# Kernel optimization log

Measured on AMD Instinct MI355X. Metric: run time of the kernel, lower is better.

The kernel has to match this reference:

```python
import jax, jax.numpy as jnp
import numpy as np

N_U, N_D = 64, 64
N_E = N_U + N_D
N_A = 32
N_SV, N_PV = 512, 64
# n1 = [4*N_A, N_SV, N_SV, N_SV]; n2 = [4, N_PV, N_PV, N_PV]


def setup_inputs() -> dict:
    key = jax.random.key(0)
    ks = jax.random.split(key, 32)
    n1 = [4 * N_A, N_SV, N_SV, N_SV]
    n2 = [4, N_PV, N_PV, N_PV]
    d = {}
    d['r'] = jax.random.normal(ks[0], (N_E, 3), jnp.float32)
    d['a'] = jax.random.normal(ks[1], (N_A, 3), jnp.float32)
    i = 2
    for l in range(3):
        fin = 3 * n1[l] + 2 * n2[l]
        d[f'V{l}_w'] = jax.random.normal(ks[i], (fin, n1[l + 1]), jnp.float32) / np.float32(np.sqrt(fin)); i += 1
        d[f'V{l}_b'] = jax.random.normal(ks[i], (n1[l + 1],), jnp.float32); i += 1
        d[f'W{l}_w'] = jax.random.normal(ks[i], (n2[l], n2[l + 1]), jnp.float32) / np.float32(np.sqrt(n2[l])); i += 1
        d[f'W{l}_b'] = jax.random.normal(ks[i], (n2[l + 1],), jnp.float32); i += 1
    fin = 3 * N_SV + 2 * N_PV
    d['after_w'] = jax.random.normal(ks[i], (fin, N_SV), jnp.float32) / np.float32(np.sqrt(fin)); i += 1
    d['after_b'] = jax.random.normal(ks[i], (N_SV,), jnp.float32); i += 1
    d['vhu_w'] = jax.random.normal(ks[i], (N_SV, N_SV // 2), jnp.float32) / np.float32(np.sqrt(N_SV)); i += 1
    d['vhu_b'] = jax.random.normal(ks[i], (N_SV // 2,), jnp.float32); i += 1
    d['vhd_w'] = jax.random.normal(ks[i], (N_SV, N_SV // 2), jnp.float32) / np.float32(np.sqrt(N_SV)); i += 1
    d['vhd_b'] = jax.random.normal(ks[i], (N_SV // 2,), jnp.float32); i += 1
    d['wu_w'] = jax.random.normal(ks[i], (N_SV // 2, N_U), jnp.float32) / np.float32(np.sqrt(N_SV // 2)); i += 1
    d['wu_b'] = jax.random.normal(ks[i], (N_U,), jnp.float32); i += 1
    d['wd_w'] = jax.random.normal(ks[i], (N_SV // 2, N_D), jnp.float32) / np.float32(np.sqrt(N_SV // 2)); i += 1
    d['wd_b'] = jax.random.normal(ks[i], (N_D,), jnp.float32); i += 1
    return d


def _fb_block(s_v, p_v):
    # s_v: (N_E, f_s), p_v: (N_E, N_E, f_p)
    s_u_mean = jnp.tile(s_v[:N_U].mean(0)[None, :], (N_E, 1))
    s_d_mean = jnp.tile(s_v[N_U:].mean(0)[None, :], (N_E, 1))
    p_u_mean = p_v[:N_U].mean(0)  # (N_E, f_p)
    p_d_mean = p_v[N_U:].mean(0)
    return jnp.concatenate([s_u_mean, s_d_mean, p_u_mean, p_d_mean, s_v], axis=-1)


def _forward(r, a, Vw, Vb, Ww, Wb, after_w, after_b, vhu_w, vhu_b, vhd_w, vhd_b, wu_w, wu_b, wd_w, wd_b):
    eye = jnp.eye(N_E, dtype=r.dtype)[:, :, None]
    ra = r[:, None, :] - a[None, :, :]                       # (N_E, N_A, 3)
    ra_len = jnp.linalg.norm(ra, axis=-1, keepdims=True)     # (N_E, N_A, 1)
    rr = r[None, :, :] - r[:, None, :]                       # (N_E, N_E, 3)
    rr_len = jnp.linalg.norm(rr + eye, axis=-1, keepdims=True) * (1.0 - eye)
    s_v = jnp.concatenate([ra, ra_len], axis=-1).reshape(N_E, -1)  # (N_E, 4*N_A)
    p_v = jnp.concatenate([rr, rr_len], axis=-1)                   # (N_E, N_E, 4)
    for vw, vb, ww, wb in zip(Vw, Vb, Ww, Wb):
        s_in = _fb_block(s_v, p_v)
        # NOTE: torch residual `s_v if s_v.shape[-1]==n_sv` never fires here:
        # fb_block output width is 3*n1+2*n2 != n_sv, so it adds zeros.
        s_v = jnp.tanh(s_in @ vw + vb)
        p_new = jnp.tanh(p_v @ ww + wb)
        p_v = p_new + (p_v if p_v.shape[-1] == N_PV else 0.0)
    s_in = _fb_block(s_v, p_v)
    s_v = jnp.tanh(s_in @ after_w + after_b)  # (N_E, N_SV); residual again never fires
    s_u = s_v[:N_U] @ vhu_w + vhu_b
    s_d = s_v[N_U:] @ vhd_w + vhd_b
    s_wu = s_u @ wu_w + wu_b   # (N_U, N_U)
    s_wd = s_d @ wd_w + wd_b   # (N_D, N_D)
    exp_u = jnp.linalg.norm(ra[:N_U], axis=-1, keepdims=True)  # (N_U, N_A, 1)
    exp_d = jnp.linalg.norm(ra[N_U:], axis=-1, keepdims=True)
    orb_u = (s_wu * jnp.exp(-exp_u).sum(axis=1))[None]  # (1, N_U, N_U)
    orb_d = (s_wd * jnp.exp(-exp_d).sum(axis=1))[None]
    # logabssumdet for two (1,n,n) matrices with n>1: no 1x1 dets.
    sgn_u, ld_u = jnp.linalg.slogdet(orb_u)
    sgn_d, ld_d = jnp.linalg.slogdet(orb_d)
    sign = sgn_u * sgn_d
    logdet = ld_u + ld_d        # (1,)
    maxlogdet = logdet.max()
    psi = (sign * jnp.exp(logdet - maxlogdet)).sum()
    return jnp.log(jnp.abs(psi)) + maxlogdet  # scalar log|psi|


def reference(r, a, V0_w, V0_b, V1_w, V1_b, V2_w, V2_b, W0_w, W0_b, W1_w, W1_b, W2_w, W2_b,
              after_w, after_b, vhu_w, vhu_b, vhd_w, vhd_b, wu_w, wu_b, wd_w, wd_b):
    Vw, Vb = [V0_w, V1_w, V2_w], [V0_b, V1_b, V2_b]
    Ww, Wb = [W0_w, W1_w, W2_w], [W0_b, W1_b, W2_b]
    return _forward(r, a, Vw, Vb, Ww, Wb, after_w, after_b,
                    vhu_w, vhu_b, vhd_w, vhd_b, wu_w, wu_b, wd_w, wd_b)
```

## Files before the change

kernel.cpp:

```cpp
#include <hip/hip_runtime.h>
#include <math.h>

#define NSV 512

__device__ void pchain_role(int b, const float* __restrict__ r,
                            const float* __restrict__ apos,
                            const float* __restrict__ W0w, const float* __restrict__ W0b,
                            const float* __restrict__ W1w, const float* __restrict__ W1b,
                            const float* __restrict__ W2w, const float* __restrict__ W2b,
                            float* __restrict__ expv,
                            float* __restrict__ pme1, float* __restrict__ pme2,
                            float* __restrict__ pme3, float* sh)
{
    float* rL    = sh;
    float* W0l   = sh + 384;
    float* aposL = sh + 640;
    float* shex  = sh + 736;
    float* p0c   = sh + 768;
    float* PA    = sh + 1024;
    float* Wbuf  = sh + 5376;
    const int j  = b >> 1, sp = b & 1;
    const int t  = threadIdx.x;
    const int i  = t >> 3;
    const int o0 = (t & 7) * 8;

    if (t < 384) rL[t] = r[t];
    else if (t < 480) aposL[t - 384] = apos[t - 384];
    for (int idx = t; idx < 4096; idx += 512) Wbuf[idx] = W1w[idx];
    if (t < 256) W0l[t] = W0w[t];
    __syncthreads();

    const float rjx = rL[j*3+0], rjy = rL[j*3+1], rjz = rL[j*3+2];
    if (t < 64) {
        const int ii = sp*64 + t;
        float dx = rjx - rL[ii*3+0], dy = rjy - rL[ii*3+1], dz = rjz - rL[ii*3+2];
        float len = (ii == j) ? 0.f : sqrtf(dx*dx + dy*dy + dz*dz);
        p0c[t*4+0]=dx; p0c[t*4+1]=dy; p0c[t*4+2]=dz; p0c[t*4+3]=len;
    } else if (sp == 0 && t < 96) {
        const int k = t - 64;
        float dx = rjx - aposL[k*3+0], dy = rjy - aposL[k*3+1], dz = rjz - aposL[k*3+2];
        shex[k] = expf(-sqrtf(dx*dx + dy*dy + dz*dz));
    }
    __syncthreads();

    {
        const float x0=p0c[i*4+0], x1=p0c[i*4+1], x2=p0c[i*4+2], x3=p0c[i*4+3];
        #pragma unroll
        for (int k = 0; k < 8; ++k) {
            const int o = o0 + k;
            float a = W0b[o];
            a = fmaf(x0, W0l[o],     a);
            a = fmaf(x1, W0l[64+o],  a);
            a = fmaf(x2, W0l[128+o], a);
            a = fmaf(x3, W0l[192+o], a);
            PA[i*68+o] = tanhf(a);
        }
    }
    if (sp == 0 && t == 4) {
        float s = 0.f;
        #pragma unroll 8
        for (int k = 0; k < 32; ++k) s += shex[k];
        expv[j] = s;
    }
    __syncthreads();

    if (t < 64) {
        float s = 0.f;
        #pragma unroll 8
        for (int k = 0; k < 64; ++k) s += PA[k*68 + t];
        pme1[j*128 + sp*64 + t] = s * 0.015625f;
    }
    float acc[8], res[8];
    const float* pa = PA + i*68;
    {
        #pragma unroll
        for (int k = 0; k < 8; ++k) acc[k] = W1b[o0+k];
        #pragma unroll 4
        for (int c = 0; c < 64; ++c) {
            const float av = pa[c];
            const float* wr = Wbuf + c*64 + o0;
            float4 wa = *reinterpret_cast<const float4*>(wr);
            float4 wb = *reinterpret_cast<const float4*>(wr+4);
            acc[0]=fmaf(av,wa.x,acc[0]); acc[1]=fmaf(av,wa.y,acc[1]);
            acc[2]=fmaf(av,wa.z,acc[2]); acc[3]=fmaf(av,wa.w,acc[3]);
            acc[4]=fmaf(av,wb.x,acc[4]); acc[5]=fmaf(av,wb.y,acc[5]);
            acc[6]=fmaf(av,wb.z,acc[6]); acc[7]=fmaf(av,wb.w,acc[7]);
        }
        #pragma unroll
        for (int k = 0; k < 8; ++k) res[k] = pa[o0+k];
    }
    __syncthreads();
    #pragma unroll
    for (int k = 0; k < 8; ++k) PA[i*68+o0+k] = tanhf(acc[k]) + res[k];
    __syncthreads();

    if (t < 64) {
        float s = 0.f;
        #pragma unroll 8
        for (int k = 0; k < 64; ++k) s += PA[k*68 + t];
        pme2[j*128 + sp*64 + t] = s * 0.015625f;
    }
    for (int idx = t; idx < 4096; idx += 512) Wbuf[idx] = W2w[idx];
    __syncthreads();

    {
        #pragma unroll
        for (int k = 0; k < 8; ++k) acc[k] = W2b[o0+k];
        #pragma unroll 4
        for (int c = 0; c < 64; ++c) {
            const float av = pa[c];
            const float* wr = Wbuf + c*64 + o0;
            float4 wa = *reinterpret_cast<const float4*>(wr);
            float4 wb = *reinterpret_cast<const float4*>(wr+4);
            acc[0]=fmaf(av,wa.x,acc[0]); acc[1]=fmaf(av,wa.y,acc[1]);
            acc[2]=fmaf(av,wa.z,acc[2]); acc[3]=fmaf(av,wa.w,acc[3]);
            acc[4]=fmaf(av,wb.x,acc[4]); acc[5]=fmaf(av,wb.y,acc[5]);
            acc[6]=fmaf(av,wb.z,acc[6]); acc[7]=fmaf(av,wb.w,acc[7]);
        }
        #pragma unroll
        for (int k = 0; k < 8; ++k) res[k] = pa[o0+k];
    }
    __syncthreads();
    #pragma unroll
    for (int k = 0; k < 8; ++k) PA[i*68+o0+k] = tanhf(acc[k]) + res[k];
    __syncthreads();

    if (t < 64) {
        float s = 0.f;
        #pragma unroll 8
        for (int k = 0; k < 64; ++k) s += PA[k*68 + t];
        pme3[j*128 + sp*64 + t] = s * 0.015625f;
    }
}

__device__ void a0_role(int ab, const float* __restrict__ r,
                        const float* __restrict__ apos,
                        const float* __restrict__ V0w, const float* __restrict__ V0b,
                        float* __restrict__ svA, float* __restrict__ psA, float* sh)
{
    constexpr int KP = 136, KP2 = 68;
    float* As    = sh;
    float* smL   = sh + 544;
    float* red   = sh + 800;
    float* t1L   = sh + 1312;
    float* rL    = sh + 1376;
    float* aposL = sh + 1760;
    const int t  = threadIdx.x;
    const int et = ab >> 3, e0 = et * 4;
    const int o0 = (ab & 7) * 64;
    const int ol = t & 63, o = o0 + ol;
    const int wv = t >> 6;

    if (t < 384) rL[t] = r[t];
    else if (t < 480) aposL[t - 384] = apos[t - 384];
    __syncthreads();

    if (t < 128) {
        const int e_l = t >> 5, k = t & 31;
        const int e = e0 + e_l;
        float dx = rL[e*3+0]-aposL[k*3+0], dy = rL[e*3+1]-aposL[k*3+1],
              dz = rL[e*3+2]-aposL[k*3+2];
        float len = sqrtf(dx*dx + dy*dy + dz*dz);
        float* dst = As + e_l*KP + 8 + k*4;
        dst[0]=dx; dst[1]=dy; dst[2]=dz; dst[3]=len;
    } else if (t < 160) {
        const int q = t - 128;
        const int e_l = q >> 3, outp = q & 7;
        const int spin = outp >> 2, c = outp & 3;
        const int e = e0 + e_l;
        const float ex = rL[e*3+0], ey = rL[e*3+1], ez = rL[e*3+2];
        float s = 0.f;
        for (int i2 = 0; i2 < 64; ++i2) {
            const int ii = spin*64 + i2;
            float dx = ex - rL[ii*3+0], dy = ey - rL[ii*3+1], dz = ez - rL[ii*3+2];
            float v = (c==0)?dx:(c==1)?dy:(c==2)?dz:
                      ((ii==e)?0.f:sqrtf(dx*dx+dy*dy+dz*dz));
            s += v;
        }
        As[e_l*KP + outp] = s * 0.015625f;
    }
    {
        const int outp = t >> 1, half = t & 1;
        const int spin = outp >> 7, cc = outp & 127, a_i = cc >> 2, d = cc & 3;
        const float ax = aposL[a_i*3+0], ay = aposL[a_i*3+1], az = aposL[a_i*3+2];
        float s = 0.f;
        #pragma unroll 8
        for (int q = 0; q < 32; ++q) {
            const int e = spin*64 + half*32 + q;
            float dx = rL[e*3+0]-ax, dy = rL[e*3+1]-ay, dz = rL[e*3+2]-az;
            float len = sqrtf(dx*dx + dy*dy + dz*dz);
            s += (d==0)?dx:(d==1)?dy:(d==2)?dz:len;
        }
        red[t] = s;
    }
    __syncthreads();
    if (t < 256) smL[t] = (red[2*t] + red[2*t+1]) * 0.015625f;
    __syncthreads();

    {
        float a1 = 0.f;
        const float* Wp = V0w + (size_t)(wv*32)*NSV + o;
        const float* mp = smL + wv*32;
        #pragma unroll 8
        for (int k = 0; k < 32; ++k) a1 = fmaf(mp[k], Wp[(size_t)k*NSV], a1);
        red[wv*64 + ol] = a1;
    }
    __syncthreads();
    if (t < 64) {
        float s = V0b[o0 + t];
        #pragma unroll
        for (int g = 0; g < 8; ++g) s += red[g*64 + t];
        t1L[t] = s;
    }
    __syncthreads();

    const int e_l = wv & 3, kh = wv >> 2;
    {
        float a2 = (kh == 0) ? t1L[ol] : 0.f;
        const float* Ap = As + e_l*KP + kh*KP2;
        const float* Wp = V0w + (size_t)(256 + kh*KP2)*NSV + o;
        #pragma unroll 16
        for (int k = 0; k < KP2; ++k)
            a2 = fmaf(Ap[k], Wp[(size_t)k*NSV], a2);
        red[wv*64 + ol] = a2;
    }
    __syncthreads();
    float v = 0.f;
    if (t < 256) {
        v = tanhf(red[(t>>6)*64 + (t&63)] + red[((t>>6)+4)*64 + (t&63)]);
        svA[(size_t)(e0 + (t>>6))*NSV + o0 + (t&63)] = v;
    }
    __syncthreads();
    if (t < 256) red[t] = v;
    __syncthreads();
    if (t < 64) {
        float s = red[t] + red[64+t] + red[128+t] + red[192+t];
        psA[(size_t)et*NSV + o0 + t] = s;
    }
}

__device__ void headc_role(int g, const float* __restrict__ vh,
                           const float* __restrict__ wu,
                           float* __restrict__ Cdst, float* sh)
{
    float* wuL = sh;
    float* vhL = sh + 4096;
    const int t = threadIdx.x;
    const int o2 = t & 63, wq = t >> 6;
    const int f0 = g * 16;
    float a0 = 0.f, a1 = 0.f;
    for (int hc = 0; hc < 4; ++hc) {
        __syncthreads();
        for (int idx = t; idx < 4096; idx += 512)
            wuL[idx] = wu[(size_t)(hc*64 + (idx>>6))*64 + (idx&63)];
        for (int idx = t; idx < 1024; idx += 512)
            vhL[idx] = vh[(size_t)(f0 + (idx>>6))*256 + hc*64 + (idx&63)];
        __syncthreads();
        #pragma unroll 8
        for (int h = 0; h < 64; ++h) {
            const float wuv = wuL[h*64 + o2];
            a0 = fmaf(vhL[wq*64 + h],     wuv, a0);
            a1 = fmaf(vhL[(wq+8)*64 + h], wuv, a1);
        }
    }
    Cdst[(size_t)(f0 + wq)*64 + o2]     = a0;
    Cdst[(size_t)(f0 + wq + 8)*64 + o2] = a1;
}

__device__ void cb_role(const float* __restrict__ vhb, const float* __restrict__ wu,
                        const float* __restrict__ wub, float* __restrict__ cbdst,
                        float* sh)
{
    const int t = threadIdx.x;
    const int o2 = t & 63, wq = t >> 6;
    float acc = 0.f;
    #pragma unroll
    for (int k = 0; k < 32; ++k) {
        const int h = wq*32 + k;
        acc = fmaf(vhb[h], wu[(size_t)h*64 + o2], acc);
    }
    sh[t] = acc;
    __syncthreads();
    if (t < 64) {
        float s = wub[t];
        #pragma unroll
        for (int g = 0; g < 8; ++g) s += sh[g*64 + t];
        cbdst[t] = s;
    }
}

__global__ __launch_bounds__(512)
void front_kernel(const float* __restrict__ r, const float* __restrict__ apos,
                  const float* __restrict__ V0w, const float* __restrict__ V0b,
                  const float* __restrict__ W0w, const float* __restrict__ W0b,
                  const float* __restrict__ W1w, const float* __restrict__ W1b,
                  const float* __restrict__ W2w, const float* __restrict__ W2b,
                  const float* __restrict__ vhuw, const float* __restrict__ vhub,
                  const float* __restrict__ vhdw, const float* __restrict__ vhdb,
                  const float* __restrict__ wuw,  const float* __restrict__ wub,
                  const float* __restrict__ wdw,  const float* __restrict__ wdb,
                  float* __restrict__ svA, float* __restrict__ expv,
                  float* __restrict__ pme1, float* __restrict__ pme2,
                  float* __restrict__ pme3, float* __restrict__ psA,
                  float* __restrict__ Cmat, float* __restrict__ cb)
{
    __shared__ __align__(16) float sh[9472];
    const int b = blockIdx.x;
    if (b < 256) {
        pchain_role(b, r, apos, W0w, W0b, W1w, W1b, W2w, W2b,
                    expv, pme1, pme2, pme3, sh);
    } else if (b < 512) {
        a0_role(b - 256, r, apos, V0w, V0b, svA, psA, sh);
    } else if (b < 576) {
        const int g = b - 512;
        const int spin = g >> 5;
        headc_role(g & 31, spin ? vhdw : vhuw, spin ? wdw : wuw,
                   Cmat + (size_t)spin*32768, sh);
    } else {
        const int spin = b - 576;
        cb_role(spin ? vhdb : vhub, spin ? wdw : wuw, spin ? wdb : wub,
                cb + spin*64, sh);
    }
}

template<int FS, int FP>
__global__ __launch_bounds__(512)
void a2_kernel(const float* __restrict__ svIn, const float* __restrict__ pmeIn,
               const float* __restrict__ psumIn,
               const float* __restrict__ Vw, const float* __restrict__ Vb,
               float* __restrict__ svOut, float* __restrict__ psumOut,
               float* __restrict__ orbInit, const float* __restrict__ cb)
{
    constexpr int KP  = 2*FP + FS;
    constexpr int KP2 = KP/2;
    __shared__ __align__(16) float As[4*KP];
    __shared__ __align__(16) float smL[2*FS];
    __shared__ __align__(16) float red[512];
    __shared__ float t1L[64];
    const int t  = threadIdx.x;
    if (blockIdx.x >= 256) {
        for (int idx = t; idx < 8192; idx += 512)
            orbInit[idx] = cb[(((idx >> 6) >> 6) << 6) + (idx & 63)];
        return;
    }
    const int et = blockIdx.x >> 3;
    const int e0 = et * 4;
    const int o0 = (blockIdx.x & 7) * 64;
    const int ol = t & 63;
    const int o  = o0 + ol;
    const int wv = t >> 6;

    for (int idx = t; idx < 4*2*FP; idx += 512)
        As[(idx/(2*FP))*KP + idx%(2*FP)] =
            pmeIn[(size_t)(e0 + idx/(2*FP))*(2*FP) + idx%(2*FP)];
    for (int idx = t; idx < FS; idx += 512) {
        const int row = idx / (FS/4), c4 = idx % (FS/4);
        *reinterpret_cast<float4*>(&As[row*KP + 2*FP + c4*4]) =
            *reinterpret_cast<const float4*>(&svIn[(size_t)(e0+row)*FS + c4*4]);
    }
    for (int idx = t; idx < 2*FS; idx += 512) {
        const int col = (idx < FS) ? idx : idx - FS;
        const int r0  = (idx < FS) ? 0 : 16;
        const float* base = psumIn + (size_t)r0*NSV + col;
        float s = 0.f;
        #pragma unroll
        for (int k = 0; k < 16; ++k) s += base[(size_t)k*NSV];
        smL[idx] = s * 0.015625f;
    }
    __syncthreads();

    {
        constexpr int TI = (2*FS)/8;
        float a1 = 0.f;
        const float* Wp = Vw + (size_t)(wv*TI)*NSV + o;
        const float* mp = smL + wv*TI;
        #pragma unroll 8
        for (int k = 0; k < TI; ++k) a1 = fmaf(mp[k], Wp[(size_t)k*NSV], a1);
        red[wv*64 + ol] = a1;
    }
    __syncthreads();
    if (t < 64) {
        float s = Vb[o0 + t];
        #pragma unroll
        for (int g = 0; g < 8; ++g) s += red[g*64 + t];
        t1L[t] = s;
    }
    __syncthreads();

    const int e_l = wv & 3, kh = wv >> 2;
    {
        float a2 = (kh == 0) ? t1L[ol] : 0.f;
        const float* Ap = As + e_l*KP + kh*KP2;
        const float* Wp = Vw + (size_t)(2*FS + kh*KP2)*NSV + o;
        #pragma unroll 16
        for (int k = 0; k < KP2; ++k)
            a2 = fmaf(Ap[k], Wp[(size_t)k*NSV], a2);
        red[wv*64 + ol] = a2;
    }
    __syncthreads();
    float v = 0.f;
    if (t < 256) {
        v = tanhf(red[(t>>6)*64 + (t&63)] + red[((t>>6)+4)*64 + (t&63)]);
        svOut[(size_t)(e0 + (t>>6))*NSV + o0 + (t&63)] = v;
    }
    if (psumOut) {
        __syncthreads();
        if (t < 256) red[t] = v;
        __syncthreads();
        if (t < 64) {
            float s = red[t] + red[64+t] + red[128+t] + red[192+t];
            psumOut[(size_t)et*NSV + o0 + t] = s;
        }
    }
}

__global__ __launch_bounds__(512)
void a3h_kernel(const float* __restrict__ svIn, const float* __restrict__ pmeIn,
                const float* __restrict__ psumIn,
                const float* __restrict__ Vw, const float* __restrict__ Vb,
                const float* __restrict__ Cmat, float* __restrict__ orb)
{
    constexpr int FS = 512, FP = 64;
    constexpr int KP  = 2*FP + FS;
    constexpr int KP2 = KP/2;
    __shared__ __align__(16) float As[4*KP];
    __shared__ __align__(16) float smL[2*FS];
    __shared__ __align__(16) float red[512];
    __shared__ float t1L[64];
    const int t  = threadIdx.x;
    const int et = blockIdx.x >> 3;
    const int e0 = et * 4;
    const int o0 = (blockIdx.x & 7) * 64;
    const int ol = t & 63;
    const int o  = o0 + ol;
    const int wv = t >> 6;

    for (int idx = t; idx < 4*2*FP; idx += 512)
        As[(idx/(2*FP))*KP + idx%(2*FP)] =
            pmeIn[(size_t)(e0 + idx/(2*FP))*(2*FP) + idx%(2*FP)];
    for (int idx = t; idx < FS; idx += 512) {
        const int row = idx / (FS/4), c4 = idx % (FS/4);
        *reinterpret_cast<float4*>(&As[row*KP + 2*FP + c4*4]) =
            *reinterpret_cast<const float4*>(&svIn[(size_t)(e0+row)*FS + c4*4]);
    }
    for (int idx = t; idx < 2*FS; idx += 512) {
        const int col = (idx < FS) ? idx : idx - FS;
        const int r0  = (idx < FS) ? 0 : 16;
        const float* base = psumIn + (size_t)r0*NSV + col;
        float s = 0.f;
        #pragma unroll
        for (int k = 0; k < 16; ++k) s += base[(size_t)k*NSV];
        smL[idx] = s * 0.015625f;
    }
    __syncthreads();

    {
        constexpr int TI = (2*FS)/8;
        float a1 = 0.f;
        const float* Wp = Vw + (size_t)(wv*TI)*NSV + o;
        const float* mp = smL + wv*TI;
        #pragma unroll 8
        for (int k = 0; k < TI; ++k) a1 = fmaf(mp[k], Wp[(size_t)k*NSV], a1);
        red[wv*64 + ol] = a1;
    }
    __syncthreads();
    if (t < 64) {
        float s = Vb[o0 + t];
        #pragma unroll
        for (int g = 0; g < 8; ++g) s += red[g*64 + t];
        t1L[t] = s;
    }
    __syncthreads();

    const int e_l = wv & 3, kh = wv >> 2;
    {
        float a2 = (kh == 0) ? t1L[ol] : 0.f;
        const float* Ap = As + e_l*KP + kh*KP2;
        const float* Wp = Vw + (size_t)(2*FS + kh*KP2)*NSV + o;
        #pragma unroll 16
        for (int k = 0; k < KP2; ++k)
            a2 = fmaf(Ap[k], Wp[(size_t)k*NSV], a2);
        red[wv*64 + ol] = a2;
    }
    __syncthreads();
    float v = 0.f;
    if (t < 256)
        v = tanhf(red[(t>>6)*64 + (t&63)] + red[((t>>6)+4)*64 + (t&63)]);
    __syncthreads();
    if (t < 256) smL[t] = v;
    __syncthreads();
    if (t < 256) {
        const int el2 = t >> 6, o2 = t & 63;
        const int spin = et >> 4;
        const float* Cp = Cmat + (size_t)spin*32768 + (size_t)o0*64 + o2;
        const float* sp = smL + el2*64;
        float acc = 0.f;
        #pragma unroll 8
        for (int f = 0; f < 64; ++f)
            acc = fmaf(sp[f], Cp[(size_t)f*64], acc);
        atomicAdd(&orb[(size_t)(e0 + el2)*64 + o2], acc);
    }
}

__device__ __forceinline__ int imax2(int a, int b) { return a > b ? a : b; }
__device__ __forceinline__ float readlane_f(float x, int lane) {
    return __int_as_float(__builtin_amdgcn_readlane(__float_as_int(x), lane));
}

__global__ __launch_bounds__(128)
void det_kernel(const float* __restrict__ orb, const float* __restrict__ expv,
                float* __restrict__ out)
{
    __shared__ float parts[2];
    const int t = threadIdx.x;
    const int w = t >> 6;
    const int lane = t & 63;
    const float* M = orb + (size_t)w*4096 + (size_t)lane*64;
    const float ex = expv[w*64 + lane];
    float rr[64];
    #pragma unroll
    for (int j = 0; j < 64; j += 4) {
        float4 v = *reinterpret_cast<const float4*>(M + j);
        rr[j]=v.x*ex; rr[j+1]=v.y*ex; rr[j+2]=v.z*ex; rr[j+3]=v.w*ex;
    }
    float pv_mine = 1.f;
    bool active = true;
    #pragma unroll
    for (int k = 0; k < 64; ++k) {
        int bits = (int)(__float_as_uint(rr[k]) & 0x7FFFFFC0u);
        int v = active ? (bits | lane) : lane;
        int tmp;
        tmp = __builtin_amdgcn_update_dpp(0, v, 0xB1,  0xF, 0xF, true); v = imax2(v, tmp);
        tmp = __builtin_amdgcn_update_dpp(0, v, 0x4E,  0xF, 0xF, true); v = imax2(v, tmp);
        tmp = __builtin_amdgcn_update_dpp(0, v, 0x141, 0xF, 0xF, true); v = imax2(v, tmp);
        tmp = __builtin_amdgcn_update_dpp(0, v, 0x140, 0xF, 0xF, true); v = imax2(v, tmp);
        tmp = __builtin_amdgcn_update_dpp(0, v, 0x142, 0xF, 0xF, true); v = imax2(v, tmp);
        tmp = __builtin_amdgcn_update_dpp(0, v, 0x143, 0xF, 0xF, true); v = imax2(v, tmp);
        const int idx = __builtin_amdgcn_readlane(v, 63) & 63;
        const float piv = readlane_f(rr[k], idx);
        pv_mine = (lane == k) ? piv : pv_mine;
        const float linv = __builtin_amdgcn_rcpf(piv);
        const float l = (active && lane != idx) ? rr[k]*linv : 0.f;
        if (lane == idx) active = false;
        #pragma unroll
        for (int j = k+1; j < 64; ++j)
            rr[j] = fmaf(-l, readlane_f(rr[j], idx), rr[j]);
    }
    float lg = logf(fabsf(pv_mine));
    #pragma unroll
    for (int off = 32; off; off >>= 1) lg += __shfl_down(lg, off);
    if (lane == 0) parts[w] = lg;
    __syncthreads();
    if (t == 0) out[0] = parts[0] + parts[1];
}

extern "C" void kernel_launch(void* const* d_in, const int* in_sizes, int n_in,
                              void* d_out, int out_size, void* d_ws, size_t ws_size,
                              hipStream_t stream)
{
    const float* r    = (const float*)d_in[0];
    const float* apos = (const float*)d_in[1];
    const float* V0w  = (const float*)d_in[2];
    const float* V0b  = (const float*)d_in[3];
    const float* W0w  = (const float*)d_in[4];
    const float* W0b  = (const float*)d_in[5];
    const float* V1w  = (const float*)d_in[6];
    const float* V1b  = (const float*)d_in[7];
    const float* W1w  = (const float*)d_in[8];
    const float* W1b  = (const float*)d_in[9];
    const float* V2w  = (const float*)d_in[10];
    const float* V2b  = (const float*)d_in[11];
    const float* W2w  = (const float*)d_in[12];
    const float* W2b  = (const float*)d_in[13];
    const float* afw  = (const float*)d_in[14];
    const float* afb  = (const float*)d_in[15];
    const float* vhuw = (const float*)d_in[16];
    const float* vhub = (const float*)d_in[17];
    const float* vhdw = (const float*)d_in[18];
    const float* vhdb = (const float*)d_in[19];
    const float* wuw  = (const float*)d_in[20];
    const float* wub  = (const float*)d_in[21];
    const float* wdw  = (const float*)d_in[22];
    const float* wdb  = (const float*)d_in[23];

    float* ws   = (float*)d_ws;
    float* svA  = ws;
    float* svB  = svA  + 65536;
    float* expv = svB  + 65536;
    float* pme1 = expv + 128;
    float* pme2 = pme1 + 16384;
    float* pme3 = pme2 + 16384;
    float* psA  = pme3 + 16384;
    float* psB  = psA  + 16384;
    float* orb  = psB  + 16384;
    float* Cmat = orb  + 8192;
    float* cb   = Cmat + 65536;

    front_kernel<<<578, 512, 0, stream>>>(r, apos, V0w, V0b, W0w, W0b,
                                          W1w, W1b, W2w, W2b,
                                          vhuw, vhub, vhdw, vhdb,
                                          wuw, wub, wdw, wdb,
                                          svA, expv, pme1, pme2, pme3, psA,
                                          Cmat, cb);
    a2_kernel<512, 64><<<257, 512, 0, stream>>>(svA, pme1, psA, V1w, V1b,
                                                svB, psB, orb, cb);
    a2_kernel<512, 64><<<256, 512, 0, stream>>>(svB, pme2, psB, V2w, V2b,
                                                svA, psA, nullptr, nullptr);
    a3h_kernel<<<256, 512, 0, stream>>>(svA, pme3, psA, afw, afb, Cmat, orb);
    det_kernel<<<1, 128, 0, stream>>>(orb, expv, (float*)d_out);
}
```

Before: 91.68 us.

## Fuse determinant into last layer kernel via last-block atomic counter

Removes the separate det_kernel launch by having every a3h block increment a global counter after its orb atomics. The last block to arrive runs the LU-based slogdet tail, reading orb through device-scope atomic loads. The counter is reset in the extra block of the first a2 kernel. This saves one kernel launch and its gap, but relies on relaxed atomics plus an explicit vmcnt wait for cross-block visibility, and the determinant now runs inside a block sized for 512 threads.

Result: slower. 94.88 us (+3.5%).

```diff
diff --git a/kernel.cpp b/kernel.cpp
--- a/kernel.cpp
+++ b/kernel.cpp
@@ -2,6 +2,12 @@
 #include <math.h>
 
 #define NSV 512
+
+__device__ __forceinline__ float2 gload2(const float* p) {
+    unsigned long long u = __hip_atomic_load((const unsigned long long*)p,
+                            __ATOMIC_RELAXED, __HIP_MEMORY_SCOPE_AGENT);
+    union { unsigned long long u; float2 f; } c; c.u = u; return c.f;
+}
 
 __device__ void pchain_role(int b, const float* __restrict__ r,
                             const float* __restrict__ apos,
@@ -329,7 +335,8 @@
                const float* __restrict__ psumIn,
                const float* __restrict__ Vw, const float* __restrict__ Vb,
                float* __restrict__ svOut, float* __restrict__ psumOut,
-               float* __restrict__ orbInit, const float* __restrict__ cb)
+               float* __restrict__ orbInit, const float* __restrict__ cb,
+               unsigned* __restrict__ cnt)
 {
     constexpr int KP  = 2*FP + FS;
     constexpr int KP2 = KP/2;
@@ -341,6 +348,9 @@
     if (blockIdx.x >= 256) {
         for (int idx = t; idx < 8192; idx += 512)
             orbInit[idx] = cb[(((idx >> 6) >> 6) << 6) + (idx & 63)];
+        if (t == 0)
+            __hip_atomic_store(cnt, 0u, __ATOMIC_RELAXED,
+                               __HIP_MEMORY_SCOPE_AGENT);
         return;
     }
     const int et = blockIdx.x >> 3;
@@ -414,11 +424,66 @@
     }
 }
 
-__global__ __launch_bounds__(512)
-void a3h_kernel(const float* __restrict__ svIn, const float* __restrict__ pmeIn,
-                const float* __restrict__ psumIn,
-                const float* __restrict__ Vw, const float* __restrict__ Vb,
-                const float* __restrict__ Cmat, float* __restrict__ orb)
+__device__ __forceinline__ int imax2(int a, int b) { return a > b ? a : b; }
+__device__ __forceinline__ float readlane_f(float x, int lane) {
+    return __int_as_float(__builtin_amdgcn_readlane(__float_as_int(x), lane));
+}
+
+__device__ void det_tail(const float* __restrict__ orb,
+                         const float* __restrict__ expv,
+                         float* __restrict__ out, float* shparts)
+{
+    const int t = threadIdx.x;
+    if (t < 128) {
+        const int w = t >> 6;
+        const int lane = t & 63;
+        const float* M = orb + (size_t)w*4096 + (size_t)lane*64;
+        const float ex = expv[w*64 + lane];
+        float rr[64];
+        #pragma unroll
+        for (int j = 0; j < 64; j += 2) {
+            float2 v = gload2(M + j);
+            rr[j] = v.x * ex; rr[j+1] = v.y * ex;
+        }
+        float pv_mine = 1.f;
+        bool active = true;
+        #pragma unroll
+        for (int k = 0; k < 64; ++k) {
+            int bits = (int)(__float_as_uint(rr[k]) & 0x7FFFFFC0u);
+            int v = active ? (bits | lane) : lane;
+            int tmp;
+            tmp = __builtin_amdgcn_update_dpp(0, v, 0xB1,  0xF, 0xF, true); v = imax2(v, tmp);
+            tmp = __builtin_amdgcn_update_dpp(0, v, 0x4E,  0xF, 0xF, true); v = imax2(v, tmp);
+            tmp = __builtin_amdgcn_update_dpp(0, v, 0x141, 0xF, 0xF, true); v = imax2(v, tmp);
+            tmp = __builtin_amdgcn_update_dpp(0, v, 0x140, 0xF, 0xF, true); v = imax2(v, tmp);
+            tmp = __builtin_amdgcn_update_dpp(0, v, 0x142, 0xF, 0xF, true); v = imax2(v, tmp);
+            tmp = __builtin_amdgcn_update_dpp(0, v, 0x143, 0xF, 0xF, true); v = imax2(v, tmp);
+            const int idx = __builtin_amdgcn_readlane(v, 63) & 63;
+            const float piv = readlane_f(rr[k], idx);
+            pv_mine = (lane == k) ? piv : pv_mine;
+            const float linv = __builtin_amdgcn_rcpf(piv);
+            const float l = (active && lane != idx) ? rr[k]*linv : 0.f;
+            if (lane == idx) active = false;
+            #pragma unroll
+            for (int j = k+1; j < 64; ++j)
+                rr[j] = fmaf(-l, readlane_f(rr[j], idx), rr[j]);
+        }
+        float lg = logf(fabsf(pv_mine));
+        #pragma unroll
+        for (int off = 32; off; off >>= 1) lg += __shfl_down(lg, off);
+        if (lane == 0) shparts[w] = lg;
+    }
+    __syncthreads();
+    if (t == 0) out[0] = shparts[0] + shparts[1];
+}
+
+__global__ __launch_bounds__(512, 1)
+void a3hd_kernel(const float* __restrict__ svIn, const float* __restrict__ pmeIn,
+                 const float* __restrict__ psumIn,
+                 const float* __restrict__ Vw, const float* __restrict__ Vb,
+                 const float* __restrict__ Cmat, float* __restrict__ orb,
+                 const float* __restrict__ expv, unsigned* __restrict__ cnt,
+                 float* __restrict__ out)
 {
     constexpr int FS = 512, FP = 64;
     constexpr int KP  = 2*FP + FS;
@@ -427,6 +492,7 @@
     __shared__ __align__(16) float smL[2*FS];
     __shared__ __align__(16) float red[512];
     __shared__ float t1L[64];
+    __shared__ unsigned lastrank;
     const int t  = threadIdx.x;
     const int et = blockIdx.x >> 3;
     const int e0 = et * 4;
@@ -500,58 +566,15 @@
             acc = fmaf(sp[f], Cp[(size_t)f*64], acc);
         atomicAdd(&orb[(size_t)(e0 + el2)*64 + o2], acc);
     }
-}
-
-__device__ __forceinline__ int imax2(int a, int b) { return a > b ? a : b; }
-__device__ __forceinline__ float readlane_f(float x, int lane) {
-    return __int_as_float(__builtin_amdgcn_readlane(__float_as_int(x), lane));
-}
-
-__global__ __launch_bounds__(128)
-void det_kernel(const float* __restrict__ orb, const float* __restrict__ expv,
-                float* __restrict__ out)
-{
-    __shared__ float parts[2];
-    const int t = threadIdx.x;
-    const int w = t >> 6;
-    const int lane = t & 63;
-    const float* M = orb + (size_t)w*4096 + (size_t)lane*64;
-    const float ex = expv[w*64 + lane];
-    float rr[64];
-    #pragma unroll
-    for (int j = 0; j < 64; j += 4) {
-        float4 v = *reinterpret_cast<const float4*>(M + j);
-        rr[j]=v.x*ex; rr[j+1]=v.y*ex; rr[j+2]=v.z*ex; rr[j+3]=v.w*ex;
-    }
-    float pv_mine = 1.f;
-    bool active = true;
-    #pragma unroll
-    for (int k = 0; k < 64; ++k) {
-        int bits = (int)(__float_as_uint(rr[k]) & 0x7FFFFFC0u);
-        int v = active ? (bits | lane) : lane;
-        int tmp;
-        tmp = __builtin_amdgcn_update_dpp(0, v, 0xB1,  0xF, 0xF, true); v = imax2(v, tmp);
-        tmp = __builtin_amdgcn_update_dpp(0, v, 0x4E,  0xF, 0xF, true); v = imax2(v, tmp);
-        tmp = __builtin_amdgcn_update_dpp(0, v, 0x141, 0xF, 0xF, true); v = imax2(v, tmp);
-        tmp = __builtin_amdgcn_update_dpp(0, v, 0x140, 0xF, 0xF, true); v = imax2(v, tmp);
-        tmp = __builtin_amdgcn_update_dpp(0, v, 0x142, 0xF, 0xF, true); v = imax2(v, tmp);
-        tmp = __builtin_amdgcn_update_dpp(0, v, 0x143, 0xF, 0xF, true); v = imax2(v, tmp);
-        const int idx = __builtin_amdgcn_readlane(v, 63) & 63;
-        const float piv = readlane_f(rr[k], idx);
-        pv_mine = (lane == k) ? piv : pv_mine;
-        const float linv = __builtin_amdgcn_rcpf(piv);
-        const float l = (active && lane != idx) ? rr[k]*linv : 0.f;
-        if (lane == idx) active = false;
-        #pragma unroll
-        for (int j = k+1; j < 64; ++j)
-            rr[j] = fmaf(-l, readlane_f(rr[j], idx), rr[j]);
-    }
-    float lg = logf(fabsf(pv_mine));
-    #pragma unroll
-    for (int off = 32; off; off >>= 1) lg += __shfl_down(lg, off);
-    if (lane == 0) parts[w] = lg;
-    __syncthreads();
-    if (t == 0) out[0] = parts[0] + parts[1];
+
+    asm volatile("s_waitcnt vmcnt(0)" ::: "memory");
+    __syncthreads();
+    if (t == 0)
+        lastrank = __hip_atomic_fetch_add(cnt, 1u, __ATOMIC_RELAXED,
+                                          __HIP_MEMORY_SCOPE_AGENT);
+    __syncthreads();
+    if (lastrank == 255u)
+        det_tail(orb, expv, out, t1L);
 }
 
 extern "C" void kernel_launch(void* const* d_in, const int* in_sizes, int n_in,
@@ -595,6 +618,7 @@
     float* orb  = psB  + 16384;
     float* Cmat = orb  + 8192;
     float* cb   = Cmat + 65536;
+    unsigned* cnt = (unsigned*)(cb + 128);
 
     front_kernel<<<578, 512, 0, stream>>>(r, apos, V0w, V0b, W0w, W0b,
                                           W1w, W1b, W2w, W2b,
@@ -603,9 +627,9 @@
                                           svA, expv, pme1, pme2, pme3, psA,
                                           Cmat, cb);
     a2_kernel<512, 64><<<257, 512, 0, stream>>>(svA, pme1, psA, V1w, V1b,
-                                                svB, psB, orb, cb);
+                                                svB, psB, orb, cb, cnt);
     a2_kernel<512, 64><<<256, 512, 0, stream>>>(svB, pme2, psB, V2w, V2b,
-                                                svA, psA, nullptr, nullptr);
-    a3h_kernel<<<256, 512, 0, stream>>>(svA, pme3, psA, afw, afb, Cmat, orb);
-    det_kernel<<<1, 128, 0, stream>>>(orb, expv, (float*)d_out);
-}
+                                                svA, psA, nullptr, nullptr, nullptr);
+    a3hd_kernel<<<256, 512, 0, stream>>>(svA, pme3, psA, afw, afb, Cmat, orb,
+                                         expv, cnt, (float*)d_out);
+}
```
